# Optimization experiments

Measured on AMD Instinct MI355X. Metric: run time of the kernel, lower is better.

Reference implementation:

```python
import jax, jax.numpy as jnp
import numpy as np
from jax import lax

MU = 3.986004418e14   # Earth GM [m^3/s^2]
A_REF = 6378136.3     # reference radius [m]


def _constants(N, dtype):
    """Precompute n1/n2 normalization tables, diagonal aBar values and the
    sub-diagonal coefficient, exactly as in compute_normalization_constants
    and the first loop of compute_aBar (these depend only on N, not on data)."""
    L = N + 2
    l = np.arange(L, dtype=np.float64)[:, None]
    m = np.arange(L, dtype=np.float64)[None, :]
    mask = l >= m + 2
    d1 = np.where(mask, (l - m) * (l + m), 1.0)
    n1 = np.where(mask, np.sqrt((2.0 * l + 1.0) * (2.0 * l - 1.0) / d1), 0.0)
    d2 = np.where(mask, (l + m) * (l - m) * (2.0 * l - 3.0), 1.0)
    num2 = np.where(mask, (l + m - 1.0) * (2.0 * l + 1.0) * (l - m - 1.0), 0.0)
    n2 = np.where(mask, np.sqrt(num2 / d2), 0.0)
    # getK(0)=1, getK(l>0)=2
    k = np.where(np.arange(L) == 0, 1.0, 2.0)
    ls = np.arange(1, L, dtype=np.float64)
    f = np.ones(L)
    f[1:] = np.sqrt((2.0 * ls + 1.0) * k[1:] / (2.0 * ls * k[:-1]))
    diag = np.cumprod(f)                  # aBar[l,l]
    sub = np.zeros(L)
    sub[1:] = np.sqrt(2.0 * ls * k[:-1] / k[1:])  # aBar[l,l-1] = sub[l]*diag[l]*u
    cast = lambda x: jnp.asarray(x, dtype=dtype)
    return cast(n1), cast(n2), cast(diag), cast(sub)


def _forward(inputs, cBar, sBar):
    N = cBar.shape[0] - 3
    L = N + 2
    dt = inputs.dtype
    r, s, t, u = inputs[:, 0], inputs[:, 1], inputs[:, 2], inputs[:, 3]
    B = r.shape[0]
    n1, n2, diag, sub = _constants(N, dt)

    # rhol[b, l] = (mu/r) * (a/r)^l  for l = 0..N  (compute_rhol)
    rho = A_REF / r
    rhol = (MU / r)[:, None] * rho[:, None] ** jnp.arange(N + 1, dtype=dt)  # [B, N+1]

    # rE[m] + i*iM[m] = (s + i t)^m, m = 0..N+1  (compute_rE_iM)
    def trig_step(c, _):
        re, im = c
        nc = (s * re - t * im, s * im + t * re)
        return nc, nc
    init = (jnp.ones_like(s), jnp.zeros_like(s))
    _, (reS, imS) = lax.scan(trig_step, init, None, length=L - 1)
    rE = jnp.concatenate([init[0][None], reS], axis=0).T  # [B, L]
    iM = jnp.concatenate([init[1][None], imS], axis=0).T  # [B, L]

    # rows of aBar for l=0 and l=1
    sqrt3 = jnp.sqrt(jnp.asarray(3.0, dt))
    row0 = jnp.zeros((B, L), dt).at[:, 0].set(1.0)
    row1 = jnp.zeros((B, L), dt).at[:, 1].set(sqrt3)
    row1 = row1.at[:, 0].set(sqrt3 * u)  # aBar[1,0] = sub[1]*diag[1]*u

    cB = cBar[:, :L].astype(dt)
    sB = sBar[:, :L].astype(dt)
    eye = jnp.eye(L, dtype=dt)

    # scan over degree l = 2..N; carry = (aBar row l-1, aBar row l-2)
    xs = (n1[2:N + 1], n2[2:N + 1], cB[2:N + 1], sB[2:N + 1],
          eye[2:N + 1], eye[1:N], diag[2:N + 1], sub[2:N + 1],
          rhol[:, 2:N + 1].T)

    def body(carry, x):
        rl1, rl2 = carry
        n1l, n2l, cl, sl, el, elm1, dl, sbl, rh = x
        # recurrence a[l,m] = u*n1[l,m]*a[l-1,m] - n2[l,m]*a[l-2,m]  (m <= l-2;
        # n1/n2 are zero elsewhere so other entries stay 0 before diag fill)
        row = u[:, None] * (n1l * rl1) - n2l * rl2
        row = row + dl * el + (sbl * dl) * u[:, None] * elm1
        contrib = rh * jnp.sum(row * (cl * rE + sl * iM), axis=1)
        return (row, rl1), contrib

    _, contribs = lax.scan(body, (row1, row0), xs)  # [N-1, B]

    pot1 = rhol[:, 1] * jnp.sum(row1 * (cB[1] * rE + sB[1] * iM), axis=1)
    potential = MU / r + pot1 + contribs.sum(axis=0)
    return (-potential)[:, None]


def setup_inputs() -> dict:
    key = jax.random.key(0)
    B, N = 65536, 64
    k1, k2, k3, k4 = jax.random.split(key, 4)
    d = jax.random.normal(k1, (B, 3), dtype=jnp.float32)
    d = d / jnp.linalg.norm(d, axis=1, keepdims=True)  # (s,t,u) direction cosines
    r = A_REF * (1.0 + jax.random.uniform(k2, (B,), dtype=jnp.float32,
                                          minval=0.05, maxval=1.0))
    inputs = jnp.concatenate([r[:, None], d], axis=1)  # [B,4] = (r,s,t,u)
    cBar = jax.random.normal(k3, (N + 3, N + 3), dtype=jnp.float32) * 1e-3
    sBar = jax.random.normal(k4, (N + 3, N + 3), dtype=jnp.float32) * 1e-3
    return {"inputs": inputs, "cBar": cBar, "sBar": sBar}


def reference(inputs, cBar, sBar):
    return _forward(inputs, cBar, sBar)
```

## Files before the change

### kernel.cpp

```cpp
#include <hip/hip_runtime.h>
#include <math.h>

#define NDEG 64
#define LMAX 66
#define LDCB 67
#define TABW 66

#define MU_F   398600441800000.0f
#define AREF_F 6378136.3f

#define NSUB 8
#define EPW  64

__global__ void pines_setup(const float* __restrict__ cBar,
                            const float* __restrict__ sBar,
                            float4* __restrict__ tab,
                            float4* __restrict__ headA,
                            float4* __restrict__ headB) {
    __shared__ float s_diag[LMAX], s_sub[LMAX];
    int t = threadIdx.x;
    if (t < LMAX) {
        double d = 1.0;
        for (int l = 1; l <= t; ++l) {
            double kp = (l == 1) ? 1.0 : 2.0;
            d *= sqrt((2.0 * l + 1.0) * 2.0 / (2.0 * l * kp));
        }
        s_diag[t] = (float)d;
        double kp = (t == 1) ? 1.0 : 2.0;
        s_sub[t] = (t == 0) ? 0.0f : (float)sqrt(2.0 * t * kp / 2.0);
    }
    __syncthreads();
    for (int m = t; m <= NDEG; m += blockDim.x) {
        float dg = s_diag[m];
        float sd = s_sub[m + 1] * s_diag[m + 1];
        headA[m] = make_float4(dg, sd, cBar[m * LDCB + m], sBar[m * LDCB + m]);
        float cb1 = (m < NDEG) ? cBar[(m + 1) * LDCB + m] : 0.0f;
        float sb1 = (m < NDEG) ? sBar[(m + 1) * LDCB + m] : 0.0f;
        headB[m] = make_float4(cb1, sb1, 0.0f, 0.0f);
    }
    for (int i = t; i < 65 * TABW; i += blockDim.x) {
        int m = i / TABW, l = i % TABW;
        if (l >= m + 2 && l <= NDEG) {
            float d1f = (float)((l - m) * (l + m));
            float v1  = sqrtf((float)((2 * l + 1) * (2 * l - 1)) / d1f);
            float d2f = (float)((l + m) * (l - m) * (2 * l - 3));
            float n2f = (float)((l + m - 1) * (2 * l + 1) * (l - m - 1));
            float v2  = sqrtf(n2f / d2f);
            tab[i] = make_float4(v1, v2, cBar[l * LDCB + m], sBar[l * LDCB + m]);
        }
    }
}

__global__ __launch_bounds__(512) void pines_kernel(
        const float4* __restrict__ inputs,
        const float4* __restrict__ tab,
        const float4* __restrict__ headA,
        const float4* __restrict__ headB,
        float* __restrict__ out, int B) {
    __shared__ float part[NSUB][EPW];

    int t = threadIdx.x;
    int j = __builtin_amdgcn_readfirstlane(t >> 6);
    int e = t & (EPW - 1);
    int elem = blockIdx.x * EPW + e;
    int lelem = elem < B ? elem : (B - 1);

    float4 in = inputs[lelem];
    float r = in.x, ss = in.y, tt = in.z, u = in.w;

    float rho  = AREF_F / r;
    float rho2 = rho * rho;
    float ur   = u * rho;

    int d1 = 15 - 2 * j;
    int d2 = 1 + 2 * j;

    auto cpow = [&](int e_, float& re_, float& im_) {
        float br = ss, bi = tt;
        re_ = 1.0f; im_ = 0.0f;
        int ee = e_;
        while (ee) {
            if (ee & 1) {
                float nr = re_ * br - im_ * bi;
                im_ = re_ * bi + im_ * br;
                re_ = nr;
            }
            float sr = br * br - bi * bi;
            bi = 2.0f * br * bi;
            br = sr;
            ee >>= 1;
        }
    };
    auto rpow = [&](int e_) {
        float b = rho, acc = 1.0f;
        int ee = e_;
        while (ee) {
            if (ee & 1) acc *= b;
            b *= b;
            ee >>= 1;
        }
        return acc;
    };

    float re, im;      cpow(j, re, im);
    float s1r, s1i;    cpow(d1, s1r, s1i);
    float s2r, s2i;    cpow(d2, s2r, s2i);
    float rstep1 = rpow(d1);
    float rstep2 = rpow(d2);
    float rho_m  = rpow(j);

    float sum = (j == 0) ? 1.0f : 0.0f;

    int m = j;
    #pragma unroll 1
    for (int k = 0; k < 8; ++k) {
        int sm = __builtin_amdgcn_readfirstlane(m);
        float4 ha = headA[sm];
        float4 hb = headB[sm];
        float q0 = ha.x * rho_m;
        float sA = (sm >= 1) ? q0 * ha.z : 0.0f;
        float sB = (sm >= 1) ? q0 * ha.w : 0.0f;
        float q1 = (ha.y * u) * (rho_m * rho);
        sA = fmaf(q1, hb.x, sA);
        sB = fmaf(q1, hb.y, sB);

        const float4* __restrict__ tp = tab + sm * TABW;
        for (int l = sm + 2; l <= NDEG; ++l) {
            float4 c = tp[l];
            float t1 = c.x * q1;
            float t2 = ur * t1;
            float t3 = c.y * q0;
            float q  = fmaf(-rho2, t3, t2);
            sA = fmaf(q, c.z, sA);
            sB = fmaf(q, c.w, sB);
            q0 = q1;
            q1 = q;
        }
        sum = fmaf(re, sA, sum);
        sum = fmaf(im, sB, sum);

        if (k & 1) {
            float nr = re * s2r - im * s2i;
            im = re * s2i + im * s2r; re = nr;
            rho_m *= rstep2; m += d2;
        } else {
            float nr = re * s1r - im * s1i;
            im = re * s1i + im * s1r; re = nr;
            rho_m *= rstep1; m += d1;
        }
    }
    if (j == 0) {
        float4 ha = headA[NDEG];
        float q0 = ha.x * rho_m;
        sum = fmaf(re * q0, ha.z, sum);
        sum = fmaf(im * q0, ha.w, sum);
    }

    part[j][e] = sum;
    __syncthreads();
    if (j == 0) {
        float tot = 0.0f;
        #pragma unroll
        for (int q = 0; q < NSUB; ++q) tot += part[q][e];
        if (elem < B) out[elem] = -(MU_F / r) * tot;
    }
}

extern "C" void kernel_launch(void* const* d_in, const int* in_sizes, int n_in,
                              void* d_out, int out_size, void* d_ws, size_t ws_size,
                              hipStream_t stream) {
    const float* inputs = (const float*)d_in[0];
    const float* cBar   = (const float*)d_in[1];
    const float* sBar   = (const float*)d_in[2];
    float* out = (float*)d_out;
    int B = in_sizes[0] / 4;

    float4* tab   = (float4*)d_ws;
    float4* headA = tab + 65 * TABW;
    float4* headB = headA + 65;

    hipLaunchKernelGGL(pines_setup, dim3(1), dim3(256), 0, stream,
                       cBar, sBar, tab, headA, headB);

    int blocks = (B + EPW - 1) / EPW;
    hipLaunchKernelGGL(pines_kernel, dim3(blocks), dim3(512), 0, stream,
                       (const float4*)inputs, tab, headA, headB, out, B);
}
```

Measured before the change: 110.1 us.

## Pack coefficient table into zero-padded 4-wide column groups with 4x unrolled recurrence

```diff
diff --git a/kernel.cpp b/kernel.cpp
--- a/kernel.cpp
+++ b/kernel.cpp
@@ -4,19 +4,22 @@
 #define NDEG 64
 #define LMAX 66
 #define LDCB 67
-#define TABW 66
+#define NCOL 63
 
 #define MU_F   398600441800000.0f
 #define AREF_F 6378136.3f
 
 #define NSUB 8
 #define EPW  64
+
+struct Cons4 { float4 v[4]; };
 
 __global__ void pines_setup(const float* __restrict__ cBar,
                             const float* __restrict__ sBar,
                             float4* __restrict__ tab,
                             float4* __restrict__ headA,
-                            float4* __restrict__ headB) {
+                            float4* __restrict__ headB,
+                            int*    __restrict__ colstart) {
     __shared__ float s_diag[LMAX], s_sub[LMAX];
     int t = threadIdx.x;
     if (t < LMAX) {
@@ -30,23 +33,35 @@
         s_sub[t] = (t == 0) ? 0.0f : (float)sqrt(2.0 * t * kp / 2.0);
     }
     __syncthreads();
-    for (int m = t; m <= NDEG; m += blockDim.x) {
-        float dg = s_diag[m];
-        float sd = s_sub[m + 1] * s_diag[m + 1];
-        headA[m] = make_float4(dg, sd, cBar[m * LDCB + m], sBar[m * LDCB + m]);
+    if (t <= NDEG) {
+        int m = t;
+        headA[m] = make_float4(s_diag[m], s_sub[m + 1] * s_diag[m + 1],
+                               cBar[m * LDCB + m], sBar[m * LDCB + m]);
         float cb1 = (m < NDEG) ? cBar[(m + 1) * LDCB + m] : 0.0f;
         float sb1 = (m < NDEG) ? sBar[(m + 1) * LDCB + m] : 0.0f;
         headB[m] = make_float4(cb1, sb1, 0.0f, 0.0f);
-    }
-    for (int i = t; i < 65 * TABW; i += blockDim.x) {
-        int m = i / TABW, l = i % TABW;
-        if (l >= m + 2 && l <= NDEG) {
-            float d1f = (float)((l - m) * (l + m));
-            float v1  = sqrtf((float)((2 * l + 1) * (2 * l - 1)) / d1f);
-            float d2f = (float)((l + m) * (l - m) * (2 * l - 3));
-            float n2f = (float)((l + m - 1) * (2 * l + 1) * (l - m - 1));
-            float v2  = sqrtf(n2f / d2f);
-            tab[i] = make_float4(v1, v2, cBar[l * LDCB + m], sBar[l * LDCB + m]);
+
+        int off = 0;
+        for (int mm = 0; mm < m && mm < NCOL; ++mm)
+            off += ((63 - mm + 3) >> 2) << 2;
+        colstart[m] = off;
+
+        if (m < NCOL) {
+            int cnt = 63 - m;
+            int pad = ((cnt + 3) >> 2) << 2;
+            for (int i = 0; i < pad; ++i) {
+                float4 v = make_float4(0.0f, 0.0f, 0.0f, 0.0f);
+                if (i < cnt) {
+                    int l = m + 2 + i;
+                    float d1f = (float)((l - m) * (l + m));
+                    float v1  = sqrtf((float)((2 * l + 1) * (2 * l - 1)) / d1f);
+                    float d2f = (float)((l + m) * (l - m) * (2 * l - 3));
+                    float n2f = (float)((l + m - 1) * (2 * l + 1) * (l - m - 1));
+                    float v2  = sqrtf(n2f / d2f);
+                    v = make_float4(v1, v2, cBar[l * LDCB + m], sBar[l * LDCB + m]);
+                }
+                tab[off + i] = v;
+            }
         }
     }
 }
@@ -56,6 +71,7 @@
         const float4* __restrict__ tab,
         const float4* __restrict__ headA,
         const float4* __restrict__ headB,
+        const int*    __restrict__ colstart,
         float* __restrict__ out, int B) {
     __shared__ float part[NSUB][EPW];
 
@@ -124,17 +140,24 @@
         sA = fmaf(q1, hb.x, sA);
         sB = fmaf(q1, hb.y, sB);
 
-        const float4* __restrict__ tp = tab + sm * TABW;
-        for (int l = sm + 2; l <= NDEG; ++l) {
-            float4 c = tp[l];
-            float t1 = c.x * q1;
-            float t2 = ur * t1;
-            float t3 = c.y * q0;
-            float q  = fmaf(-rho2, t3, t2);
-            sA = fmaf(q, c.z, sA);
-            sB = fmaf(q, c.w, sB);
-            q0 = q1;
-            q1 = q;
+        int scol = __builtin_amdgcn_readfirstlane(colstart[sm]);
+        int ng   = __builtin_amdgcn_readfirstlane((63 - sm + 3) >> 2);
+        const Cons4* __restrict__ gp = (const Cons4*)(tab + scol);
+        #pragma unroll 1
+        for (int g = 0; g < ng; ++g) {
+            Cons4 c = gp[g];
+            #pragma unroll
+            for (int q4 = 0; q4 < 4; ++q4) {
+                float4 cc = c.v[q4];
+                float t1 = cc.x * q1;
+                float t2 = ur * t1;
+                float t3 = cc.y * q0;
+                float q  = fmaf(-rho2, t3, t2);
+                sA = fmaf(q, cc.z, sA);
+                sB = fmaf(q, cc.w, sB);
+                q0 = q1;
+                q1 = q;
+            }
         }
         sum = fmaf(re, sA, sum);
         sum = fmaf(im, sB, sum);
@@ -176,13 +199,15 @@
     int B = in_sizes[0] / 4;
 
     float4* tab   = (float4*)d_ws;
-    float4* headA = tab + 65 * TABW;
+    float4* headA = tab + 4032;
     float4* headB = headA + 65;
-
-    hipLaunchKernelGGL(pines_setup, dim3(1), dim3(256), 0, stream,
-                       cBar, sBar, tab, headA, headB);
+    int*    colst = (int*)(headB + 65);
+
+    hipLaunchKernelGGL(pines_setup, dim3(1), dim3(128), 0, stream,
+                       cBar, sBar, tab, headA, headB, colst);
 
     int blocks = (B + EPW - 1) / EPW;
     hipLaunchKernelGGL(pines_kernel, dim3(blocks), dim3(512), 0, stream,
-                       (const float4*)inputs, tab, headA, headB, out, B);
+                       (const float4*)inputs, tab, headA, headB, colst,
+                       out, B);
 }
```

After: 106.8 us. 3.0% less time.

## Rescale recurrence to fold n1 into coefficients and stream per-wave padded tables

Applied to the files above, without the earlier changes.

```diff
diff --git a/kernel.cpp b/kernel.cpp
--- a/kernel.cpp
+++ b/kernel.cpp
@@ -2,60 +2,99 @@
 #include <math.h>
 
 #define NDEG 64
-#define LMAX 66
 #define LDCB 67
-#define TABW 66
 
 #define MU_F   398600441800000.0f
 #define AREF_F 6378136.3f
 
 #define NSUB 8
 #define EPW  64
+#define SGRP 72
+#define NREC 9
+
+struct Cons4 { float4 v[4]; };
+
+__device__ __forceinline__ double n1d(int l, int m) {
+    return sqrt((2.0 * l + 1.0) * (2.0 * l - 1.0) / ((double)(l - m) * (l + m)));
+}
+__device__ __forceinline__ double n2d(int l, int m) {
+    return sqrt(((double)(l + m - 1) * (2 * l + 1) * (l - m - 1)) /
+                ((double)(l + m) * (l - m) * (2 * l - 3)));
+}
 
 __global__ void pines_setup(const float* __restrict__ cBar,
                             const float* __restrict__ sBar,
-                            float4* __restrict__ tab,
-                            float4* __restrict__ headA,
-                            float4* __restrict__ headB) {
-    __shared__ float s_diag[LMAX], s_sub[LMAX];
-    int t = threadIdx.x;
-    if (t < LMAX) {
-        double d = 1.0;
-        for (int l = 1; l <= t; ++l) {
-            double kp = (l == 1) ? 1.0 : 2.0;
-            d *= sqrt((2.0 * l + 1.0) * 2.0 / (2.0 * l * kp));
-        }
-        s_diag[t] = (float)d;
-        double kp = (t == 1) ? 1.0 : 2.0;
-        s_sub[t] = (t == 0) ? 0.0f : (float)sqrt(2.0 * t * kp / 2.0);
-    }
-    __syncthreads();
-    for (int m = t; m <= NDEG; m += blockDim.x) {
-        float dg = s_diag[m];
-        float sd = s_sub[m + 1] * s_diag[m + 1];
-        headA[m] = make_float4(dg, sd, cBar[m * LDCB + m], sBar[m * LDCB + m]);
-        float cb1 = (m < NDEG) ? cBar[(m + 1) * LDCB + m] : 0.0f;
-        float sb1 = (m < NDEG) ? sBar[(m + 1) * LDCB + m] : 0.0f;
-        headB[m] = make_float4(cb1, sb1, 0.0f, 0.0f);
-    }
-    for (int i = t; i < 65 * TABW; i += blockDim.x) {
-        int m = i / TABW, l = i % TABW;
-        if (l >= m + 2 && l <= NDEG) {
-            float d1f = (float)((l - m) * (l + m));
-            float v1  = sqrtf((float)((2 * l + 1) * (2 * l - 1)) / d1f);
-            float d2f = (float)((l + m) * (l - m) * (2 * l - 3));
-            float n2f = (float)((l + m - 1) * (2 * l + 1) * (l - m - 1));
-            float v2  = sqrtf(n2f / d2f);
-            tab[i] = make_float4(v1, v2, cBar[l * LDCB + m], sBar[l * LDCB + m]);
-        }
-    }
-}
-
-__global__ __launch_bounds__(512) void pines_kernel(
+                            float4* __restrict__ stream,
+                            float4* __restrict__ hrec) {
+    int tid = blockIdx.x * blockDim.x + threadIdx.x;
+    if (tid < 8 * SGRP * 4) {
+        int j = tid / (SGRP * 4);
+        int rem = tid % (SGRP * 4);
+        int d1 = 15 - 2 * j, d2 = 1 + 2 * j;
+        int m = j, base = 0, idx = -1;
+        for (int k = 0; k < 8; ++k) {
+            int len  = 63 - m;
+            int ecap = ((len + 7) >> 3) << 3;
+            if (rem < base + ecap) { idx = rem - base; break; }
+            base += ecap;
+            m += (k & 1) ? d2 : d1;
+        }
+        float4 v = make_float4(0.0f, 0.0f, 0.0f, 0.0f);
+        if (idx >= 0) {
+            int l = m + 2 + idx;
+            if (l <= NDEG) {
+                double g = 1.0;
+                for (int t2 = m + 2; t2 <= l; ++t2) g *= n1d(t2, m);
+                double nn1   = n1d(l, m);
+                double nprev = (l - 1 >= m + 2) ? n1d(l - 1, m) : 1.0;
+                double nt2   = n2d(l, m) / (nn1 * nprev);
+                v = make_float4((float)nt2,
+                                (float)(g * (double)cBar[l * LDCB + m]),
+                                (float)(g * (double)sBar[l * LDCB + m]),
+                                0.0f);
+            }
+        }
+        stream[tid] = v;
+    } else {
+        int h = tid - 8 * SGRP * 4;
+        if (h < 8 * NREC) {
+            int j = h / NREC, k = h % NREC;
+            int d1 = 15 - 2 * j, d2 = 1 + 2 * j;
+            int m = j;
+            for (int kk = 0; kk < k; ++kk) m += (kk & 1) ? d2 : d1;
+            float4 a = make_float4(0.0f, 0.0f, 0.0f, 0.0f);
+            float4 b = make_float4(0.0f, 0.0f, 0.0f, 0.0f);
+            if (m <= NDEG) {
+                double diag = 1.0;
+                for (int l = 1; l <= m; ++l) {
+                    double kp = (l == 1) ? 1.0 : 2.0;
+                    diag *= sqrt((2.0 * l + 1.0) * 2.0 / (2.0 * l * kp));
+                }
+                double sd = 0.0;
+                if (m < NDEG) {
+                    double kprev = (m == 0) ? 1.0 : 2.0;
+                    double f    = sqrt((2.0 * (m + 1) + 1.0) * 2.0 /
+                                       (2.0 * (m + 1) * kprev));
+                    double sub1 = sqrt((double)(m + 1) * kprev);
+                    sd = sub1 * diag * f;
+                }
+                float cmm = (m >= 1) ? cBar[m * LDCB + m] : 0.0f;
+                float smm = (m >= 1) ? sBar[m * LDCB + m] : 0.0f;
+                float cb1 = (m < NDEG) ? cBar[(m + 1) * LDCB + m] : 0.0f;
+                float sb1 = (m < NDEG) ? sBar[(m + 1) * LDCB + m] : 0.0f;
+                a = make_float4((float)diag, (float)sd, cmm, smm);
+                b = make_float4(cb1, sb1, 0.0f, 0.0f);
+            }
+            hrec[h * 2]     = a;
+            hrec[h * 2 + 1] = b;
+        }
+    }
+}
+
+__global__ __launch_bounds__(512, 8) void pines_kernel(
         const float4* __restrict__ inputs,
-        const float4* __restrict__ tab,
-        const float4* __restrict__ headA,
-        const float4* __restrict__ headB,
+        const float4* __restrict__ stream,
+        const float4* __restrict__ hrec,
         float* __restrict__ out, int B) {
     __shared__ float part[NSUB][EPW];
 
@@ -68,9 +107,10 @@
     float4 in = inputs[lelem];
     float r = in.x, ss = in.y, tt = in.z, u = in.w;
 
-    float rho  = AREF_F / r;
-    float rho2 = rho * rho;
-    float ur   = u * rho;
+    float rho   = AREF_F / r;
+    float rho2  = rho * rho;
+    float nrho2 = -rho2;
+    float ur    = u * rho;
 
     int d1 = 15 - 2 * j;
     int d2 = 1 + 2 * j;
@@ -111,30 +151,52 @@
 
     float sum = (j == 0) ? 1.0f : 0.0f;
 
-    int m = j;
+    const float4* __restrict__ hp = hrec + j * NREC * 2;
+    const Cons4*  __restrict__ sp = (const Cons4*)stream + j * SGRP;
+
+    float4 h0 = hp[0];
+    float4 h1 = hp[1];
+
+    int m = j, g = 0;
     #pragma unroll 1
     for (int k = 0; k < 8; ++k) {
         int sm = __builtin_amdgcn_readfirstlane(m);
-        float4 ha = headA[sm];
-        float4 hb = headB[sm];
-        float q0 = ha.x * rho_m;
-        float sA = (sm >= 1) ? q0 * ha.z : 0.0f;
-        float sB = (sm >= 1) ? q0 * ha.w : 0.0f;
-        float q1 = (ha.y * u) * (rho_m * rho);
-        sA = fmaf(q1, hb.x, sA);
-        sB = fmaf(q1, hb.y, sB);
-
-        const float4* __restrict__ tp = tab + sm * TABW;
-        for (int l = sm + 2; l <= NDEG; ++l) {
-            float4 c = tp[l];
-            float t1 = c.x * q1;
-            float t2 = ur * t1;
-            float t3 = c.y * q0;
-            float q  = fmaf(-rho2, t3, t2);
-            sA = fmaf(q, c.z, sA);
-            sB = fmaf(q, c.w, sB);
-            q0 = q1;
-            q1 = q;
+        float4 h0n = hp[2 * k + 2];
+        float4 h1n = hp[2 * k + 3];
+
+        float q0 = h0.x * rho_m;
+        float sA = q0 * h0.z;
+        float sB = q0 * h0.w;
+        float q1 = (h0.y * u) * (rho_m * rho);
+        sA = fmaf(q1, h1.x, sA);
+        sB = fmaf(q1, h1.y, sB);
+
+        int ntr = __builtin_amdgcn_readfirstlane((63 - sm + 7) >> 3);
+        #pragma unroll 1
+        for (int tr = 0; tr < ntr; ++tr) {
+            Cons4 ca = sp[g];
+            Cons4 cb = sp[g + 1];
+            g += 2;
+            #pragma unroll
+            for (int q4 = 0; q4 < 4; ++q4) {
+                float4 cc = ca.v[q4];
+                float t3 = cc.x * q0;
+                float t4 = nrho2 * t3;
+                float q  = fmaf(ur, q1, t4);
+                sA = fmaf(q, cc.y, sA);
+                sB = fmaf(q, cc.z, sB);
+                q0 = q1; q1 = q;
+            }
+            #pragma unroll
+            for (int q4 = 0; q4 < 4; ++q4) {
+                float4 cc = cb.v[q4];
+                float t3 = cc.x * q0;
+                float t4 = nrho2 * t3;
+                float q  = fmaf(ur, q1, t4);
+                sA = fmaf(q, cc.y, sA);
+                sB = fmaf(q, cc.z, sB);
+                q0 = q1; q1 = q;
+            }
         }
         sum = fmaf(re, sA, sum);
         sum = fmaf(im, sB, sum);
@@ -148,12 +210,12 @@
             im = re * s1i + im * s1r; re = nr;
             rho_m *= rstep1; m += d1;
         }
-    }
-    if (j == 0) {
-        float4 ha = headA[NDEG];
-        float q0 = ha.x * rho_m;
-        sum = fmaf(re * q0, ha.z, sum);
-        sum = fmaf(im * q0, ha.w, sum);
+        h0 = h0n; h1 = h1n;
+    }
+    {
+        float q0 = h0.x * rho_m;
+        sum = fmaf(re * q0, h0.z, sum);
+        sum = fmaf(im * q0, h0.w, sum);
     }
 
     part[j][e] = sum;
@@ -168,21 +230,20 @@
 
 extern "C" void kernel_launch(void* const* d_in, const int* in_sizes, int n_in,
                               void* d_out, int out_size, void* d_ws, size_t ws_size,
-                              hipStream_t stream) {
+                              hipStream_t stream_h) {
     const float* inputs = (const float*)d_in[0];
     const float* cBar   = (const float*)d_in[1];
     const float* sBar   = (const float*)d_in[2];
     float* out = (float*)d_out;
     int B = in_sizes[0] / 4;
 
-    float4* tab   = (float4*)d_ws;
-    float4* headA = tab + 65 * TABW;
-    float4* headB = headA + 65;
-
-    hipLaunchKernelGGL(pines_setup, dim3(1), dim3(256), 0, stream,
-                       cBar, sBar, tab, headA, headB);
+    float4* strm = (float4*)d_ws;
+    float4* hrec = strm + 8 * SGRP * 4;
+
+    hipLaunchKernelGGL(pines_setup, dim3(10), dim3(256), 0, stream_h,
+                       cBar, sBar, strm, hrec);
 
     int blocks = (B + EPW - 1) / EPW;
-    hipLaunchKernelGGL(pines_kernel, dim3(blocks), dim3(512), 0, stream,
-                       (const float4*)inputs, tab, headA, headB, out, B);
-}
+    hipLaunchKernelGGL(pines_kernel, dim3(blocks), dim3(512), 0, stream_h,
+                       (const float4*)inputs, strm, hrec, out, B);
+}
```

Result: faster. 98.36 us (-10.6%).
